# Optimization experiments

Measured on AMD Instinct MI355X. Metric: run time of the kernel, lower is better.

## Reference

```python
import jax, jax.numpy as jnp
import numpy as np
from jax import lax

PATCH = 7
F_CH = 32      # args.F: adaConv output channels
N_FEATS = 64   # args.n_feats
F_HEAD = 64    # args.f
SCALE = 2
RGB_RANGE = 255.0
RGB_MEAN = jnp.array([0.4488, 0.4371, 0.4040], dtype=jnp.float32) * RGB_RANGE  # MeanShift, std=1


def _conv(x, w, b, padding):
    # x: NCHW, w: OIHW
    y = lax.conv_general_dilated(x, w, (1, 1), padding,
                                 dimension_numbers=('NCHW', 'OIHW', 'NCHW'))
    return y + b[None, :, None, None]


def _forward(x, w1, b1, w2, b2, wk, bk, wb, bb, w3, b3, w4, b4):
    B, C, H, W = x.shape
    x = x - RGB_MEAN[None, :, None, None]          # sub_mean
    # ---- Space2Batch(patch=7): pad to multiple of 7, patches -> batch dim ----
    pad_h = (-H) % PATCH
    pad_w = (-W) % PATCH
    xp = jnp.pad(x, ((0, 0), (0, 0), (0, pad_h), (0, pad_w)))
    Hp, Wp = H + pad_h, W + pad_w
    gh, gw = Hp // PATCH, Wp // PATCH
    patches = xp.reshape(B, C, gh, PATCH, gw, PATCH)
    patches = patches.transpose(0, 2, 4, 1, 3, 5).reshape(-1, C, PATCH, PATCH)  # (Bp,3,7,7)
    Bp = patches.shape[0]
    # ---- head: two valid 3x3 convs + ReLU -> (Bp, f, 3, 3) ----
    feat = jax.nn.relu(_conv(patches, w1, b1, 'VALID'))
    feat = jax.nn.relu(_conv(feat, w2, b2, 'VALID'))
    # ---- per-patch kernel / bias prediction (valid 3x3 -> 1x1 spatial) ----
    kern = _conv(feat, wk, bk, 'VALID').reshape(Bp, F_CH, 27)  # (F, Cin*kh*kw) per patch
    bias = _conv(feat, wb, bb, 'VALID').reshape(Bp, F_CH)
    # ---- adaConv: distinct predicted 3x3x3 kernel per patch, padding=1 ----
    xpad = jnp.pad(patches, ((0, 0), (0, 0), (1, 1), (1, 1)))
    # im2col ordered (C, kh, kw) to match torch kernel.view(-1, F, 3, 3, 3) flattening
    cols = jnp.stack([xpad[:, :, i:i + PATCH, j:j + PATCH]
                      for i in range(3) for j in range(3)], axis=2)  # (Bp, C, 9, 7, 7)
    cols = cols.reshape(Bp, C * 9, PATCH, PATCH)                    # (Bp, 27, 7, 7)
    y = jnp.einsum('bkhw,bfk->bfhw', cols, kern) + bias[:, :, None, None]  # (Bp, F, 7, 7)
    # ---- Batch2Space ----
    y = y.reshape(B, gh, gw, F_CH, PATCH, PATCH)
    y = y.transpose(0, 3, 1, 4, 2, 5).reshape(B, F_CH, Hp, Wp)
    # ---- body: conv5x5 F->n_feats + ReLU, conv3x3 n_feats -> 3*scale^2 ----
    y = jax.nn.relu(_conv(y, w3, b3, [(2, 2), (2, 2)]))
    y = _conv(y, w4, b4, [(1, 1), (1, 1)])
    # ---- PixelShuffle(scale) ----
    Bc, Cc, Hc, Wc = y.shape
    Co = Cc // (SCALE * SCALE)
    y = y.reshape(Bc, Co, SCALE, SCALE, Hc, Wc)
    y = y.transpose(0, 1, 4, 2, 5, 3).reshape(Bc, Co, Hc * SCALE, Wc * SCALE)
    y = y[..., :H * SCALE, :W * SCALE]
    return y + RGB_MEAN[None, :, None, None]       # add_mean


def setup_inputs() -> dict:
    key = jax.random.key(0)
    ks = jax.random.split(key, 8)

    def w(k, shape):
        fan_in = shape[1] * shape[2] * shape[3]
        return (jax.random.normal(k, shape, jnp.float32) / np.sqrt(fan_in)).astype(jnp.float32)

    f, Fc, n = F_HEAD, F_CH, N_FEATS
    return {
        'x': jax.random.uniform(ks[0], (4, 3, 360, 640), jnp.float32) * RGB_RANGE,
        'w1': w(ks[1], (f, 3, 3, 3)), 'b1': jnp.zeros((f,), jnp.float32),
        'w2': w(ks[2], (f, f, 3, 3)), 'b2': jnp.zeros((f,), jnp.float32),
        'wk': w(ks[3], (27 * Fc, f, 3, 3)), 'bk': jnp.zeros((27 * Fc,), jnp.float32),
        'wb': w(ks[4], (Fc, f, 3, 3)), 'bb': jnp.zeros((Fc,), jnp.float32),
        'w3': w(ks[5], (n, Fc, 5, 5)), 'b3': jnp.zeros((n,), jnp.float32),
        'w4': w(ks[6], (3 * SCALE * SCALE, n, 3, 3)), 'b4': jnp.zeros((3 * SCALE * SCALE,), jnp.float32),
    }


def reference(x, w1, b1, w2, b2, wk, bk, wb, bb, w3, b3, w4, b4):
    return _forward(x, w1, b1, w2, b2, wk, bk, wb, bb, w3, b3, w4, b4)
```

## Files before the change

kernel.cpp:

```cpp
#include <hip/hip_runtime.h>
#include <hip/hip_bf16.h>

#define GH 52
#define GW 92
#define BP 19136
#define HP 364
#define WP 644
#define HIN 360
#define WIN_ 640

typedef __attribute__((ext_vector_type(8))) short short8;
typedef __attribute__((ext_vector_type(4))) float f32x4;

__device__ __constant__ float c_mean[3] = {114.444f, 111.4605f, 103.02f};

#define OFF_FEAT1 0ULL
#define OFF_FEAT2 61235200ULL
#define OFF_KB    83279872ULL
#define OFF_Y64   0ULL
#define OFF_Y32   151863296ULL
#define OFF_BMG   211869696ULL
#define OFF_W1T   211873280ULL
#define OFF_W2B   211880192ULL
#define OFF_WKB   211953920ULL
#define OFF_W3B   212986112ULL
#define OFF_W4B   213088512ULL
#define WS_NEED   213106944ULL

static __device__ __forceinline__ short bf16bits(float v) {
    __hip_bfloat16 h = __float2bfloat16(v);
    return *reinterpret_cast<short*>(&h);
}

__global__ __launch_bounds__(256) void k_prep(
    const float* __restrict__ w1, float* __restrict__ w1t,
    const float* __restrict__ w2, short* __restrict__ w2b,
    const float* __restrict__ wk, const float* __restrict__ wb, short* __restrict__ wkb,
    const float* __restrict__ bk, const float* __restrict__ bb, float* __restrict__ bmg,
    const float* __restrict__ w3, short* __restrict__ w3b,
    const float* __restrict__ w4, short* __restrict__ w4b)
{
    int i = blockIdx.x * 256 + threadIdx.x;
    if (i < 1728) { int oc = i / 27, k = i % 27; w1t[k*64 + oc] = w1[i]; }
    if (i < 896)  { bmg[i] = (i < 864) ? bk[i] : bb[i - 864]; }
    if (i < 36864) {
        int c = i & 63; int rest = i >> 6; int oc = rest & 63; int tap = rest >> 6;
        int ky = tap / 3, kx = tap % 3;
        w2b[i] = bf16bits(w2[((oc*64 + c)*3 + ky)*3 + kx]);
    }
    if (i < 516096) {
        int n = i / 576, r = i % 576;
        int po = r >> 6, f = r & 63;
        int ks = f*9 + po;
        float v = (n < 864) ? wk[n*576 + ks] : wb[(n - 864)*576 + ks];
        wkb[i] = bf16bits(v);
    }
    if (i < 51200) {
        int c = i & 31; int rest = i >> 5; int oc = rest & 63; int tap = rest >> 6;
        int ky = tap / 5, kx = tap % 5;
        w3b[i] = bf16bits(w3[((oc*32 + c)*5 + ky)*5 + kx]);
    }
    if (i < 9216) {
        int c = i & 31; int rest = i >> 5; int n = rest & 15; rest >>= 4;
        int kh = rest & 1; int tap = rest >> 1;
        int ky = tap / 3, kx = tap % 3;
        float v = 0.f;
        if (n < 12) v = w4[((n*64 + kh*32 + c)*3 + ky)*3 + kx];
        w4b[i] = bf16bits(v);
    }
}

__global__ __launch_bounds__(256) void k_conv1(
    const float* __restrict__ x, const float* __restrict__ w1t, const float* __restrict__ b1,
    short* __restrict__ feat1)
{
    __shared__ float sp[16][148];
    const int tid = threadIdx.x;
    const int p0 = blockIdx.x * 16;

    for (int t = tid; t < 16*147; t += 256) {
        int p = t / 147, r = t % 147;
        int c = r / 49, rr = r % 49;
        int i = rr / 7, j = rr % 7;
        int pg = p0 + p;
        int b = pg / (GH*GW), rem = pg % (GH*GW);
        int gy = rem / GW, gx = rem % GW;
        int yy = gy*7 + i, xx = gx*7 + j;
        float v = 0.f;
        if (yy < HIN && xx < WIN_) v = x[((b*3 + c)*HIN + yy)*WIN_ + xx] - c_mean[c];
        sp[p][r] = v;
    }
    __syncthreads();

    for (int t = tid; t < 3200; t += 256) {
        int ocg = t & 7, p = (t >> 3) & 15, pos = t >> 7;
        int pi = pos / 5, pj = pos % 5;
        float acc[8];
        #pragma unroll
        for (int u = 0; u < 8; ++u) acc[u] = b1[ocg*8 + u];
        #pragma unroll
        for (int c = 0; c < 3; ++c)
            #pragma unroll
            for (int ki = 0; ki < 3; ++ki)
                #pragma unroll
                for (int kj = 0; kj < 3; ++kj) {
                    float fv = sp[p][c*49 + (pi+ki)*7 + (pj+kj)];
                    const float* wr = w1t + (c*9 + ki*3 + kj)*64 + ocg*8;
                    const float4 wa = *reinterpret_cast<const float4*>(wr);
                    const float4 wb4 = *reinterpret_cast<const float4*>(wr + 4);
                    acc[0] += fv*wa.x;  acc[1] += fv*wa.y;  acc[2] += fv*wa.z;  acc[3] += fv*wa.w;
                    acc[4] += fv*wb4.x; acc[5] += fv*wb4.y; acc[6] += fv*wb4.z; acc[7] += fv*wb4.w;
                }
        short8 pack;
        #pragma unroll
        for (int u = 0; u < 8; ++u) pack[u] = bf16bits(fmaxf(acc[u], 0.f));
        *reinterpret_cast<short8*>(feat1 + (size_t)pos*(BP*64) + (size_t)(p0 + p)*64 + ocg*8) = pack;
    }
}

__global__ __launch_bounds__(256) void k_conv2(
    const short* __restrict__ feat1, const short* __restrict__ w2b,
    const float* __restrict__ b2, short* __restrict__ feat2)
{
    const int tid = threadIdx.x;
    const int wv = tid >> 6, lane = tid & 63;
    const int n16 = lane & 15, q = lane >> 4;
    const int po = blockIdx.y;
    const int pi = po / 3, pj = po % 3;
    const int p0 = blockIdx.x * 128 + wv * 32;

    f32x4 acc[4][2];
    #pragma unroll
    for (int j = 0; j < 4; ++j) {
        float4 bj = *reinterpret_cast<const float4*>(b2 + j*16 + q*4);
        f32x4 bi = {bj.x, bj.y, bj.z, bj.w};
        acc[j][0] = bi; acc[j][1] = bi;
    }

    for (int ki = 0; ki < 3; ++ki)
        for (int kj = 0; kj < 3; ++kj) {
            const int tap = ki*3 + kj;
            const size_t base = (size_t)((pi+ki)*5 + (pj+kj)) * (BP*64);
            #pragma unroll
            for (int ks = 0; ks < 2; ++ks) {
                short8 af[4];
                #pragma unroll
                for (int j = 0; j < 4; ++j)
                    af[j] = *reinterpret_cast<const short8*>(w2b + (tap*64 + j*16 + n16)*64 + ks*32 + q*8);
                short8 bf[2];
                #pragma unroll
                for (int nt = 0; nt < 2; ++nt) {
                    int pr = p0 + nt*16 + n16; pr = (pr < BP) ? pr : (BP-1);
                    bf[nt] = *reinterpret_cast<const short8*>(feat1 + base + (size_t)pr*64 + ks*32 + q*8);
                }
                #pragma unroll
                for (int j = 0; j < 4; ++j)
                    #pragma unroll
                    for (int nt = 0; nt < 2; ++nt)
                        acc[j][nt] = __builtin_amdgcn_mfma_f32_16x16x32_bf16(af[j], bf[nt], acc[j][nt], 0, 0, 0);
            }
        }

    #pragma unroll
    for (int nt = 0; nt < 2; ++nt) {
        int pr = p0 + nt*16 + n16;
        if (pr >= BP) continue;
        #pragma unroll
        for (int j = 0; j < 4; ++j) {
            short4 pk;
            pk.x = bf16bits(fmaxf(acc[j][nt][0], 0.f));
            pk.y = bf16bits(fmaxf(acc[j][nt][1], 0.f));
            pk.z = bf16bits(fmaxf(acc[j][nt][2], 0.f));
            pk.w = bf16bits(fmaxf(acc[j][nt][3], 0.f));
            *reinterpret_cast<short4*>(feat2 + (size_t)po*(BP*64) + (size_t)pr*64 + j*16 + q*4) = pk;
        }
    }
}

__global__ __launch_bounds__(256) void k_gemm(
    const short* __restrict__ feat2, const short* __restrict__ wkb,
    const float* __restrict__ bmg, float* __restrict__ kb)
{
    __shared__ __align__(16) short As[128*40];
    __shared__ __align__(16) short Bs[128*40];
    const int tid = threadIdx.x;
    const int p0 = blockIdx.x * 128, n0 = blockIdx.y * 128;
    const int wv = tid >> 6, lane = tid & 63;
    const int n16 = lane & 15, q = lane >> 4;
    const int wm = wv & 1, wn = wv >> 1;

    f32x4 acc[4][4] = {};

    for (int k0 = 0; k0 < 576; k0 += 32) {
        const int po = k0 >> 6, cb = k0 & 63;
        for (int t = tid; t < 512; t += 256) {
            int row = t >> 2, seg = t & 3;
            uint4 a = *reinterpret_cast<const uint4*>(wkb + (size_t)(n0 + row)*576 + k0 + seg*8);
            int pr = p0 + row; pr = (pr < BP) ? pr : (BP-1);
            uint4 b = *reinterpret_cast<const uint4*>(feat2 + (size_t)po*(BP*64) + (size_t)pr*64 + cb + seg*8);
            *reinterpret_cast<uint4*>(&As[row*40 + seg*8]) = a;
            *reinterpret_cast<uint4*>(&Bs[row*40 + seg*8]) = b;
        }
        __syncthreads();
        short8 af[4], bf[4];
        #pragma unroll
        for (int mt = 0; mt < 4; ++mt)
            af[mt] = *reinterpret_cast<const short8*>(&As[(wm*64 + mt*16 + n16)*40 + q*8]);
        #pragma unroll
        for (int nt = 0; nt < 4; ++nt)
            bf[nt] = *reinterpret_cast<const short8*>(&Bs[(wn*64 + nt*16 + n16)*40 + q*8]);
        #pragma unroll
        for (int mt = 0; mt < 4; ++mt)
            #pragma unroll
            for (int nt = 0; nt < 4; ++nt)
                acc[mt][nt] = __builtin_amdgcn_mfma_f32_16x16x32_bf16(af[mt], bf[nt], acc[mt][nt], 0, 0, 0);
        __syncthreads();
    }

    #pragma unroll
    for (int nt = 0; nt < 4; ++nt) {
        int pr = p0 + wn*64 + nt*16 + n16;
        if (pr >= BP) continue;
        #pragma unroll
        for (int mt = 0; mt < 4; ++mt) {
            int nb = n0 + wm*64 + mt*16 + q*4;
            float4 bs = *reinterpret_cast<const float4*>(bmg + nb);
            float4 v;
            v.x = acc[mt][nt][0] + bs.x;
            v.y = acc[mt][nt][1] + bs.y;
            v.z = acc[mt][nt][2] + bs.z;
            v.w = acc[mt][nt][3] + bs.w;
            *reinterpret_cast<float4*>(kb + (size_t)pr*896 + nb) = v;
        }
    }
}

__global__ __launch_bounds__(256) void k_apply(
    const float* __restrict__ x, const float* __restrict__ kb, __hip_bfloat16* __restrict__ y32)
{
    __shared__ float pp[3][9][9];
    __shared__ __align__(16) float kl[27][32];
    __shared__ float bl[32];
    const int p = blockIdx.x;
    const int tid = threadIdx.x;
    const int b = p / (GH*GW), rem = p % (GH*GW);
    const int gy = rem / GW, gx = rem % GW;

    for (int t = tid; t < 243; t += 256) ((float*)pp)[t] = 0.f;
    __syncthreads();
    for (int t = tid; t < 147; t += 256) {
        int c = t / 49, r = t % 49, i = r / 7, j = r % 7;
        int yy = gy*7 + i, xx = gx*7 + j;
        float v = 0.f;
        if (yy < HIN && xx < WIN_) v = x[((b*3 + c)*HIN + yy)*WIN_ + xx] - c_mean[c];
        pp[c][i+1][j+1] = v;
    }
    for (int t = tid; t < 864; t += 256) {
        int f = t / 27, k = t % 27;
        kl[k][f] = kb[(size_t)p*896 + f*27 + k];
    }
    if (tid < 32) bl[tid] = kb[(size_t)p*896 + 864 + tid];
    __syncthreads();

    if (tid < 196) {
        int pos = tid % 49, fg = tid / 49;
        int h = pos / 7, w = pos % 7;
        float win[27];
        #pragma unroll
        for (int c = 0; c < 3; ++c)
            #pragma unroll
            for (int i = 0; i < 3; ++i)
                #pragma unroll
                for (int j = 0; j < 3; ++j)
                    win[c*9 + i*3 + j] = pp[c][h+i][w+j];
        float acc[8];
        #pragma unroll
        for (int u = 0; u < 8; ++u) acc[u] = bl[fg*8 + u];
        #pragma unroll
        for (int k = 0; k < 27; ++k) {
            const float4 wa = *reinterpret_cast<const float4*>(&kl[k][fg*8]);
            const float4 wb4 = *reinterpret_cast<const float4*>(&kl[k][fg*8 + 4]);
            float v = win[k];
            acc[0] += v*wa.x;  acc[1] += v*wa.y;  acc[2] += v*wa.z;  acc[3] += v*wa.w;
            acc[4] += v*wb4.x; acc[5] += v*wb4.y; acc[6] += v*wb4.z; acc[7] += v*wb4.w;
        }
        int yy = gy*7 + h, xx = gx*7 + w;
        short8 pack;
        #pragma unroll
        for (int u = 0; u < 8; ++u) pack[u] = bf16bits(acc[u]);
        *reinterpret_cast<short8*>(
            reinterpret_cast<short*>(y32) + (((size_t)b*HP + yy)*WP + xx)*32 + fg*8) = pack;
    }
}

__global__ __launch_bounds__(256) void k_conv3(
    const __hip_bfloat16* __restrict__ y32, const short* __restrict__ w3b,
    const float* __restrict__ b3, __hip_bfloat16* __restrict__ y64)
{
    __shared__ __align__(16) short sin_[20*20*40];
    const int tid = threadIdx.x;
    const int x0 = blockIdx.x * 16, y0 = blockIdx.y * 16, b = blockIdx.z;

    for (int t = tid; t < 1600; t += 256) {
        int pix = t >> 2, q4 = t & 3;
        int iy = pix / 20, ix = pix % 20;
        int yy = y0 + iy - 2, xx = x0 + ix - 2;
        uint4 v = make_uint4(0u, 0u, 0u, 0u);
        if (yy >= 0 && yy < HP && xx >= 0 && xx < WP)
            v = *reinterpret_cast<const uint4*>(
                reinterpret_cast<const short*>(y32) + (((size_t)b*HP + yy)*WP + xx)*32 + q4*8);
        *reinterpret_cast<uint4*>(&sin_[pix*40 + q4*8]) = v;
    }
    __syncthreads();

    const int wv = tid >> 6;
    const int lane = tid & 63;
    const int n16 = lane & 15;
    const int q = lane >> 4;

    f32x4 acc[4][4];
    #pragma unroll
    for (int j = 0; j < 4; ++j) {
        float4 bj = *reinterpret_cast<const float4*>(b3 + j*16 + q*4);
        f32x4 bi = {bj.x, bj.y, bj.z, bj.w};
        #pragma unroll
        for (int i = 0; i < 4; ++i) acc[i][j] = bi;
    }

    for (int ky = 0; ky < 5; ++ky) {
        for (int kx = 0; kx < 5; ++kx) {
            const int tap = ky*5 + kx;
            short8 afw[4];
            #pragma unroll
            for (int j = 0; j < 4; ++j)
                afw[j] = *reinterpret_cast<const short8*>(w3b + (tap*64 + j*16 + n16)*32 + q*8);
            short8 bfa[4];
            #pragma unroll
            for (int i = 0; i < 4; ++i) {
                int pix = (wv*4 + i + ky)*20 + (n16 + kx);
                bfa[i] = *reinterpret_cast<const short8*>(&sin_[pix*40 + q*8]);
            }
            #pragma unroll
            for (int i = 0; i < 4; ++i)
                #pragma unroll
                for (int j = 0; j < 4; ++j)
                    acc[i][j] = __builtin_amdgcn_mfma_f32_16x16x32_bf16(afw[j], bfa[i], acc[i][j], 0, 0, 0);
        }
    }

    const int xx = x0 + n16;
    if (xx < WP) {
        #pragma unroll
        for (int i = 0; i < 4; ++i) {
            int yy = y0 + wv*4 + i;
            if (yy >= HP) continue;
            short* dst = reinterpret_cast<short*>(y64) + (((size_t)b*HP + yy)*WP + xx)*64;
            #pragma unroll
            for (int j = 0; j < 4; ++j) {
                short4 pk;
                pk.x = bf16bits(fmaxf(acc[i][j][0], 0.f));
                pk.y = bf16bits(fmaxf(acc[i][j][1], 0.f));
                pk.z = bf16bits(fmaxf(acc[i][j][2], 0.f));
                pk.w = bf16bits(fmaxf(acc[i][j][3], 0.f));
                *reinterpret_cast<short4*>(dst + j*16 + q*4) = pk;
            }
        }
    }
}

__global__ __launch_bounds__(256) void k_conv4(
    const __hip_bfloat16* __restrict__ y64, const short* __restrict__ w4b,
    const float* __restrict__ b4, float* __restrict__ out)
{
    __shared__ __align__(16) short sin_[18*18*72];
    const int tid = threadIdx.x;
    const int x0 = blockIdx.x * 16, y0 = blockIdx.y * 16, b = blockIdx.z;

    for (int t = tid; t < 2592; t += 256) {
        int pix = t >> 3, sub = t & 7;
        int iy = pix / 18, ix = pix % 18;
        int yy = y0 + iy - 1, xx = x0 + ix - 1;
        uint4 v = make_uint4(0u, 0u, 0u, 0u);
        if (yy >= 0 && yy < HP && xx >= 0 && xx < WP)
            v = *reinterpret_cast<const uint4*>(
                reinterpret_cast<const short*>(y64) + (((size_t)b*HP + yy)*WP + xx)*64 + sub*8);
        *reinterpret_cast<uint4*>(&sin_[pix*72 + sub*8]) = v;
    }
    __syncthreads();

    const int wv = tid >> 6;
    const int lane = tid & 63;
    const int n16 = lane & 15;
    const int q = lane >> 4;

    f32x4 acc[4];
    {
        f32x4 bi = {0.f, 0.f, 0.f, 0.f};
        if (q < 3) {
            float4 bq = *reinterpret_cast<const float4*>(b4 + q*4);
            bi = {bq.x, bq.y, bq.z, bq.w};
        }
        #pragma unroll
        for (int i = 0; i < 4; ++i) acc[i] = bi;
    }

    for (int ky = 0; ky < 3; ++ky) {
        for (int kx = 0; kx < 3; ++kx) {
            const int tap = ky*3 + kx;
            short8 af0 = *reinterpret_cast<const short8*>(w4b + ((tap*2 + 0)*16 + n16)*32 + q*8);
            short8 af1 = *reinterpret_cast<const short8*>(w4b + ((tap*2 + 1)*16 + n16)*32 + q*8);
            #pragma unroll
            for (int i = 0; i < 4; ++i) {
                int pix = (wv*4 + i + ky)*18 + (n16 + kx);
                short8 a0 = *reinterpret_cast<const short8*>(&sin_[pix*72 + q*8]);
                short8 a1 = *reinterpret_cast<const short8*>(&sin_[pix*72 + 32 + q*8]);
                acc[i] = __builtin_amdgcn_mfma_f32_16x16x32_bf16(af0, a0, acc[i], 0, 0, 0);
                acc[i] = __builtin_amdgcn_mfma_f32_16x16x32_bf16(af1, a1, acc[i], 0, 0, 0);
            }
        }
    }

    if (q < 3) {
        const int xx = x0 + n16;
        const float m = c_mean[q];
        #pragma unroll
        for (int i = 0; i < 4; ++i) {
            int yy = y0 + wv*4 + i;
            if (yy >= HIN) continue;
            size_t r0 = ((size_t)(b*3 + q)*720 + yy*2)*1280 + xx*2;
            float2 s0 = {acc[i][0] + m, acc[i][1] + m};
            float2 s1 = {acc[i][2] + m, acc[i][3] + m};
            *reinterpret_cast<float2*>(out + r0) = s0;
            *reinterpret_cast<float2*>(out + r0 + 1280) = s1;
        }
    }
}

extern "C" void kernel_launch(void* const* d_in, const int* in_sizes, int n_in,
                              void* d_out, int out_size, void* d_ws, size_t ws_size,
                              hipStream_t stream) {
    const float* x  = (const float*)d_in[0];
    const float* w1 = (const float*)d_in[1];
    const float* b1 = (const float*)d_in[2];
    const float* w2 = (const float*)d_in[3];
    const float* b2 = (const float*)d_in[4];
    const float* wk = (const float*)d_in[5];
    const float* bk = (const float*)d_in[6];
    const float* wb = (const float*)d_in[7];
    const float* bb = (const float*)d_in[8];
    const float* w3 = (const float*)d_in[9];
    const float* b3 = (const float*)d_in[10];
    const float* w4 = (const float*)d_in[11];
    const float* b4 = (const float*)d_in[12];
    float* out = (float*)d_out;

    if (ws_size < WS_NEED) return;

    char* ws = (char*)d_ws;
    short* feat1 = (short*)(ws + OFF_FEAT1);
    short* feat2 = (short*)(ws + OFF_FEAT2);
    float* kb    = (float*)(ws + OFF_KB);
    __hip_bfloat16* y32 = (__hip_bfloat16*)(ws + OFF_Y32);
    __hip_bfloat16* y64 = (__hip_bfloat16*)(ws + OFF_Y64);
    float* bmg = (float*)(ws + OFF_BMG);
    float* w1t = (float*)(ws + OFF_W1T);
    short* w2b = (short*)(ws + OFF_W2B);
    short* wkb = (short*)(ws + OFF_WKB);
    short* w3b = (short*)(ws + OFF_W3B);
    short* w4b = (short*)(ws + OFF_W4B);

    k_prep <<<2016, 256, 0, stream>>>(w1, w1t, w2, w2b, wk, wb, wkb, bk, bb, bmg, w3, w3b, w4, w4b);
    k_conv1<<<BP/16, 256, 0, stream>>>(x, w1t, b1, feat1);
    k_conv2<<<dim3(150, 9), 256, 0, stream>>>(feat1, w2b, b2, feat2);
    k_gemm <<<dim3(150, 7), 256, 0, stream>>>(feat2, wkb, bmg, kb);
    k_apply<<<BP, 256, 0, stream>>>(x, kb, y32);
    k_conv3<<<dim3(41, 23, 4), 256, 0, stream>>>(y32, w3b, b3, y64);
    k_conv4<<<dim3(40, 23, 4), 256, 0, stream>>>(y64, w4b, b4, out);
}
```

Before: 522.0 us.

## Store predicted kernels in bf16 and read padded activations directly in convs

The predicted per-patch kernels are now written as bf16 in a transposed k-major layout, so the apply kernel can copy them with one vector load instead of a strided fp32 gather. The intermediate activations are stored in zero-bordered padded buffers, with small kernels that zero only the halos. This lets conv3 and conv4 drop their shared-memory staging, bounds checks and barriers and load MFMA operands straight from global memory. The aim is less traffic and fewer syncs, at the cost of bf16 rounding of the predicted kernels and redundant uncached global reads across taps.

Result: slower. 679.0 us (+30.1%).

```diff
diff --git a/kernel.cpp b/kernel.cpp
--- a/kernel.cpp
+++ b/kernel.cpp
@@ -9,27 +9,36 @@
 #define HIN 360
 #define WIN_ 640
 
+#define Y32H 368
+#define Y32W 648
+#define Y64H 365
+#define Y64W 645
+
 typedef __attribute__((ext_vector_type(8))) short short8;
 typedef __attribute__((ext_vector_type(4))) float f32x4;
 
 __device__ __constant__ float c_mean[3] = {114.444f, 111.4605f, 103.02f};
 
+#define OFF_Y64P  0ULL
 #define OFF_FEAT1 0ULL
 #define OFF_FEAT2 61235200ULL
-#define OFF_KB    83279872ULL
-#define OFF_Y64   0ULL
-#define OFF_Y32   151863296ULL
-#define OFF_BMG   211869696ULL
-#define OFF_W1T   211873280ULL
-#define OFF_W2B   211880192ULL
-#define OFF_WKB   211953920ULL
-#define OFF_W3B   212986112ULL
-#define OFF_W4B   213088512ULL
-#define WS_NEED   213106944ULL
+#define OFF_KB2   83279872ULL
+#define OFF_Y32P  120537600ULL
+#define OFF_BMG   181592576ULL
+#define OFF_W1T   181596160ULL
+#define OFF_W2B   181603072ULL
+#define OFF_WKB   181676800ULL
+#define OFF_W3B   182708992ULL
+#define OFF_W4B   182811392ULL
+#define WS_NEED   182833920ULL
 
 static __device__ __forceinline__ short bf16bits(float v) {
     __hip_bfloat16 h = __float2bfloat16(v);
     return *reinterpret_cast<short*>(&h);
+}
+static __device__ __forceinline__ float bits2f(short s) {
+    __hip_bfloat16 h = *reinterpret_cast<__hip_bfloat16*>(&s);
+    return __bfloat162float(h);
 }
 
 __global__ __launch_bounds__(256) void k_prep(
@@ -42,7 +51,9 @@
 {
     int i = blockIdx.x * 256 + threadIdx.x;
     if (i < 1728) { int oc = i / 27, k = i % 27; w1t[k*64 + oc] = w1[i]; }
-    if (i < 896)  { bmg[i] = (i < 864) ? bk[i] : bb[i - 864]; }
+    if (i < 896) {
+        bmg[i] = (i < 864) ? bk[(i & 31)*27 + (i >> 5)] : bb[i - 864];
+    }
     if (i < 36864) {
         int c = i & 63; int rest = i >> 6; int oc = rest & 63; int tap = rest >> 6;
         int ky = tap / 3, kx = tap % 3;
@@ -52,7 +63,9 @@
         int n = i / 576, r = i % 576;
         int po = r >> 6, f = r & 63;
         int ks = f*9 + po;
-        float v = (n < 864) ? wk[n*576 + ks] : wb[(n - 864)*576 + ks];
+        float v;
+        if (n < 864) { int fch = n & 31, k27 = n >> 5; v = wk[(fch*27 + k27)*576 + ks]; }
+        else v = wb[(n - 864)*576 + ks];
         wkb[i] = bf16bits(v);
     }
     if (i < 51200) {
@@ -68,6 +81,38 @@
         if (n < 12) v = w4[((n*64 + kh*32 + c)*3 + ky)*3 + kx];
         w4b[i] = bf16bits(v);
     }
+}
+
+__global__ __launch_bounds__(256) void k_zg32(short* __restrict__ y32p)
+{
+    int u = blockIdx.x * 256 + threadIdx.x;
+    if (u >= 64768) return;
+    int b = u / 16192, r = u % 16192;
+    int pxi = r >> 2, sub = r & 3;
+    int row, col;
+    if (pxi < 1296)      { row = pxi / 648;        col = pxi % 648; }
+    else if (pxi < 2592) { row = 366 + (pxi-1296)/648; col = (pxi-1296) % 648; }
+    else {
+        int s = pxi - 2592;
+        row = 2 + (s >> 2);
+        int c4 = s & 3;
+        col = (c4 < 2) ? c4 : (644 + c4);
+    }
+    uint4 z = make_uint4(0u,0u,0u,0u);
+    *reinterpret_cast<uint4*>(y32p + (((size_t)b*Y32H + row)*Y32W + col)*32 + sub*8) = z;
+}
+
+__global__ __launch_bounds__(256) void k_zg64(short* __restrict__ y64p)
+{
+    int u = blockIdx.x * 256 + threadIdx.x;
+    if (u >= 32288) return;
+    int b = u / 8072, r = u % 8072;
+    int pxi = r >> 3, sub = r & 7;
+    int row, col;
+    if (pxi < 645) { row = 0; col = pxi; }
+    else           { row = pxi - 645 + 1; col = 0; }
+    uint4 z = make_uint4(0u,0u,0u,0u);
+    *reinterpret_cast<uint4*>(y64p + (((size_t)b*Y64H + row)*Y64W + col)*64 + sub*8) = z;
 }
 
 __global__ __launch_bounds__(256) void k_conv1(
@@ -179,7 +224,7 @@
 
 __global__ __launch_bounds__(256) void k_gemm(
     const short* __restrict__ feat2, const short* __restrict__ wkb,
-    const float* __restrict__ bmg, float* __restrict__ kb)
+    const float* __restrict__ bmg, short* __restrict__ kb2)
 {
     __shared__ __align__(16) short As[128*40];
     __shared__ __align__(16) short Bs[128*40];
@@ -225,28 +270,30 @@
         for (int mt = 0; mt < 4; ++mt) {
             int nb = n0 + wm*64 + mt*16 + q*4;
             float4 bs = *reinterpret_cast<const float4*>(bmg + nb);
-            float4 v;
-            v.x = acc[mt][nt][0] + bs.x;
-            v.y = acc[mt][nt][1] + bs.y;
-            v.z = acc[mt][nt][2] + bs.z;
-            v.w = acc[mt][nt][3] + bs.w;
-            *reinterpret_cast<float4*>(kb + (size_t)pr*896 + nb) = v;
+            short4 pk;
+            pk.x = bf16bits(acc[mt][nt][0] + bs.x);
+            pk.y = bf16bits(acc[mt][nt][1] + bs.y);
+            pk.z = bf16bits(acc[mt][nt][2] + bs.z);
+            pk.w = bf16bits(acc[mt][nt][3] + bs.w);
+            *reinterpret_cast<short4*>(kb2 + (size_t)pr*896 + nb) = pk;
         }
     }
 }
 
 __global__ __launch_bounds__(256) void k_apply(
-    const float* __restrict__ x, const float* __restrict__ kb, __hip_bfloat16* __restrict__ y32)
+    const float* __restrict__ x, const short* __restrict__ kb2, short* __restrict__ y32p)
 {
     __shared__ float pp[3][9][9];
-    __shared__ __align__(16) float kl[27][32];
-    __shared__ float bl[32];
+    __shared__ __align__(16) short klb[896];
     const int p = blockIdx.x;
     const int tid = threadIdx.x;
     const int b = p / (GH*GW), rem = p % (GH*GW);
     const int gy = rem / GW, gx = rem % GW;
 
     for (int t = tid; t < 243; t += 256) ((float*)pp)[t] = 0.f;
+    if (tid < 112)
+        *reinterpret_cast<uint4*>(&klb[tid*8]) =
+            *reinterpret_cast<const uint4*>(kb2 + (size_t)p*896 + tid*8);
     __syncthreads();
     for (int t = tid; t < 147; t += 256) {
         int c = t / 49, r = t % 49, i = r / 7, j = r % 7;
@@ -255,11 +302,6 @@
         if (yy < HIN && xx < WIN_) v = x[((b*3 + c)*HIN + yy)*WIN_ + xx] - c_mean[c];
         pp[c][i+1][j+1] = v;
     }
-    for (int t = tid; t < 864; t += 256) {
-        int f = t / 27, k = t % 27;
-        kl[k][f] = kb[(size_t)p*896 + f*27 + k];
-    }
-    if (tid < 32) bl[tid] = kb[(size_t)p*896 + 864 + tid];
     __syncthreads();
 
     if (tid < 196) {
@@ -275,48 +317,33 @@
                     win[c*9 + i*3 + j] = pp[c][h+i][w+j];
         float acc[8];
         #pragma unroll
-        for (int u = 0; u < 8; ++u) acc[u] = bl[fg*8 + u];
+        for (int u = 0; u < 8; ++u) acc[u] = bits2f(klb[864 + fg*8 + u]);
         #pragma unroll
         for (int k = 0; k < 27; ++k) {
-            const float4 wa = *reinterpret_cast<const float4*>(&kl[k][fg*8]);
-            const float4 wb4 = *reinterpret_cast<const float4*>(&kl[k][fg*8 + 4]);
             float v = win[k];
-            acc[0] += v*wa.x;  acc[1] += v*wa.y;  acc[2] += v*wa.z;  acc[3] += v*wa.w;
-            acc[4] += v*wb4.x; acc[5] += v*wb4.y; acc[6] += v*wb4.z; acc[7] += v*wb4.w;
+            short8 wr = *reinterpret_cast<const short8*>(&klb[k*32 + fg*8]);
+            #pragma unroll
+            for (int u = 0; u < 8; ++u) acc[u] += v * bits2f(wr[u]);
         }
         int yy = gy*7 + h, xx = gx*7 + w;
         short8 pack;
         #pragma unroll
         for (int u = 0; u < 8; ++u) pack[u] = bf16bits(acc[u]);
         *reinterpret_cast<short8*>(
-            reinterpret_cast<short*>(y32) + (((size_t)b*HP + yy)*WP + xx)*32 + fg*8) = pack;
+            y32p + (((size_t)b*Y32H + yy + 2)*Y32W + xx + 2)*32 + fg*8) = pack;
     }
 }
 
 __global__ __launch_bounds__(256) void k_conv3(
-    const __hip_bfloat16* __restrict__ y32, const short* __restrict__ w3b,
-    const float* __restrict__ b3, __hip_bfloat16* __restrict__ y64)
-{
-    __shared__ __align__(16) short sin_[20*20*40];
-    const int tid = threadIdx.x;
-    const int x0 = blockIdx.x * 16, y0 = blockIdx.y * 16, b = blockIdx.z;
-
-    for (int t = tid; t < 1600; t += 256) {
-        int pix = t >> 2, q4 = t & 3;
-        int iy = pix / 20, ix = pix % 20;
-        int yy = y0 + iy - 2, xx = x0 + ix - 2;
-        uint4 v = make_uint4(0u, 0u, 0u, 0u);
-        if (yy >= 0 && yy < HP && xx >= 0 && xx < WP)
-            v = *reinterpret_cast<const uint4*>(
-                reinterpret_cast<const short*>(y32) + (((size_t)b*HP + yy)*WP + xx)*32 + q4*8);
-        *reinterpret_cast<uint4*>(&sin_[pix*40 + q4*8]) = v;
-    }
-    __syncthreads();
-
-    const int wv = tid >> 6;
-    const int lane = tid & 63;
-    const int n16 = lane & 15;
-    const int q = lane >> 4;
+    const short* __restrict__ y32p, const short* __restrict__ w3b,
+    const float* __restrict__ b3, short* __restrict__ y64p)
+{
+    const int tid = threadIdx.x;
+    const int wv = tid >> 6, lane = tid & 63;
+    const int n16 = lane & 15, q = lane >> 4;
+    const int x0 = blockIdx.x * 16, y0 = blockIdx.y * 16 + wv * 4, b = blockIdx.z;
+    const short* src = y32p + (size_t)b * Y32H * Y32W * 32;
+    const int cx = x0 + n16;
 
     f32x4 acc[4][4];
     #pragma unroll
@@ -328,6 +355,7 @@
     }
 
     for (int ky = 0; ky < 5; ++ky) {
+        #pragma unroll
         for (int kx = 0; kx < 5; ++kx) {
             const int tap = ky*5 + kx;
             short8 afw[4];
@@ -337,8 +365,8 @@
             short8 bfa[4];
             #pragma unroll
             for (int i = 0; i < 4; ++i) {
-                int pix = (wv*4 + i + ky)*20 + (n16 + kx);
-                bfa[i] = *reinterpret_cast<const short8*>(&sin_[pix*40 + q*8]);
+                int ry = y0 + i + ky; ry = (ry < Y32H) ? ry : (Y32H - 1);
+                bfa[i] = *reinterpret_cast<const short8*>(src + ((size_t)ry*Y32W + cx + kx)*32 + q*8);
             }
             #pragma unroll
             for (int i = 0; i < 4; ++i)
@@ -348,13 +376,13 @@
         }
     }
 
-    const int xx = x0 + n16;
-    if (xx < WP) {
+    const int ox = x0 + n16;
+    if (ox < WP) {
         #pragma unroll
         for (int i = 0; i < 4; ++i) {
-            int yy = y0 + wv*4 + i;
-            if (yy >= HP) continue;
-            short* dst = reinterpret_cast<short*>(y64) + (((size_t)b*HP + yy)*WP + xx)*64;
+            int oy = y0 + i;
+            if (oy >= HP) continue;
+            short* dst = y64p + (((size_t)b*Y64H + oy + 1)*Y64W + ox + 1)*64;
             #pragma unroll
             for (int j = 0; j < 4; ++j) {
                 short4 pk;
@@ -369,29 +397,15 @@
 }
 
 __global__ __launch_bounds__(256) void k_conv4(
-    const __hip_bfloat16* __restrict__ y64, const short* __restrict__ w4b,
+    const short* __restrict__ y64p, const short* __restrict__ w4b,
     const float* __restrict__ b4, float* __restrict__ out)
 {
-    __shared__ __align__(16) short sin_[18*18*72];
-    const int tid = threadIdx.x;
-    const int x0 = blockIdx.x * 16, y0 = blockIdx.y * 16, b = blockIdx.z;
-
-    for (int t = tid; t < 2592; t += 256) {
-        int pix = t >> 3, sub = t & 7;
-        int iy = pix / 18, ix = pix % 18;
-        int yy = y0 + iy - 1, xx = x0 + ix - 1;
-        uint4 v = make_uint4(0u, 0u, 0u, 0u);
-        if (yy >= 0 && yy < HP && xx >= 0 && xx < WP)
-            v = *reinterpret_cast<const uint4*>(
-                reinterpret_cast<const short*>(y64) + (((size_t)b*HP + yy)*WP + xx)*64 + sub*8);
-        *reinterpret_cast<uint4*>(&sin_[pix*72 + sub*8]) = v;
-    }
-    __syncthreads();
-
-    const int wv = tid >> 6;
-    const int lane = tid & 63;
-    const int n16 = lane & 15;
-    const int q = lane >> 4;
+    const int tid = threadIdx.x;
+    const int wv = tid >> 6, lane = tid & 63;
+    const int n16 = lane & 15, q = lane >> 4;
+    const int x0 = blockIdx.x * 16, y0 = blockIdx.y * 16 + wv * 4, b = blockIdx.z;
+    const short* src = y64p + (size_t)b * Y64H * Y64W * 64;
+    const int cx = x0 + n16;
 
     f32x4 acc[4];
     {
@@ -405,15 +419,17 @@
     }
 
     for (int ky = 0; ky < 3; ++ky) {
+        #pragma unroll
         for (int kx = 0; kx < 3; ++kx) {
             const int tap = ky*3 + kx;
             short8 af0 = *reinterpret_cast<const short8*>(w4b + ((tap*2 + 0)*16 + n16)*32 + q*8);
             short8 af1 = *reinterpret_cast<const short8*>(w4b + ((tap*2 + 1)*16 + n16)*32 + q*8);
             #pragma unroll
             for (int i = 0; i < 4; ++i) {
-                int pix = (wv*4 + i + ky)*18 + (n16 + kx);
-                short8 a0 = *reinterpret_cast<const short8*>(&sin_[pix*72 + q*8]);
-                short8 a1 = *reinterpret_cast<const short8*>(&sin_[pix*72 + 32 + q*8]);
+                int ry = y0 + i + ky; ry = (ry < Y64H) ? ry : (Y64H - 1);
+                const short* pr = src + ((size_t)ry*Y64W + cx + kx)*64;
+                short8 a0 = *reinterpret_cast<const short8*>(pr + q*8);
+                short8 a1 = *reinterpret_cast<const short8*>(pr + 32 + q*8);
                 acc[i] = __builtin_amdgcn_mfma_f32_16x16x32_bf16(af0, a0, acc[i], 0, 0, 0);
                 acc[i] = __builtin_amdgcn_mfma_f32_16x16x32_bf16(af1, a1, acc[i], 0, 0, 0);
             }
@@ -425,7 +441,7 @@
         const float m = c_mean[q];
         #pragma unroll
         for (int i = 0; i < 4; ++i) {
-            int yy = y0 + wv*4 + i;
+            int yy = y0 + i;
             if (yy >= HIN) continue;
             size_t r0 = ((size_t)(b*3 + q)*720 + yy*2)*1280 + xx*2;
             float2 s0 = {acc[i][0] + m, acc[i][1] + m};
@@ -459,9 +475,9 @@
     char* ws = (char*)d_ws;
     short* feat1 = (short*)(ws + OFF_FEAT1);
     short* feat2 = (short*)(ws + OFF_FEAT2);
-    float* kb    = (float*)(ws + OFF_KB);
-    __hip_bfloat16* y32 = (__hip_bfloat16*)(ws + OFF_Y32);
-    __hip_bfloat16* y64 = (__hip_bfloat16*)(ws + OFF_Y64);
+    short* kb2   = (short*)(ws + OFF_KB2);
+    short* y32p  = (short*)(ws + OFF_Y32P);
+    short* y64p  = (short*)(ws + OFF_Y64P);
     float* bmg = (float*)(ws + OFF_BMG);
     float* w1t = (float*)(ws + OFF_W1T);
     short* w2b = (short*)(ws + OFF_W2B);
@@ -470,10 +486,12 @@
     short* w4b = (short*)(ws + OFF_W4B);
 
     k_prep <<<2016, 256, 0, stream>>>(w1, w1t, w2, w2b, wk, wb, wkb, bk, bb, bmg, w3, w3b, w4, w4b);
+    k_zg32 <<<254, 256, 0, stream>>>(y32p);
     k_conv1<<<BP/16, 256, 0, stream>>>(x, w1t, b1, feat1);
     k_conv2<<<dim3(150, 9), 256, 0, stream>>>(feat1, w2b, b2, feat2);
-    k_gemm <<<dim3(150, 7), 256, 0, stream>>>(feat2, wkb, bmg, kb);
-    k_apply<<<BP, 256, 0, stream>>>(x, kb, y32);
-    k_conv3<<<dim3(41, 23, 4), 256, 0, stream>>>(y32, w3b, b3, y64);
-    k_conv4<<<dim3(40, 23, 4), 256, 0, stream>>>(y64, w4b, b4, out);
-}
+    k_gemm <<<dim3(150, 7), 256, 0, stream>>>(feat2, wkb, bmg, kb2);
+    k_apply<<<BP, 256, 0, stream>>>(x, kb2, y32p);
+    k_zg64 <<<127, 256, 0, stream>>>(y64p);
+    k_conv3<<<dim3(41, 23, 4), 256, 0, stream>>>(y32p, w3b, b3, y64p);
+    k_conv4<<<dim3(40, 23, 4), 256, 0, stream>>>(y64p, w4b, b4, out);
+}
```
